# Kernel optimization log

Hardware: AMD Instinct MI355X
Metric: run time of the kernel (lower is better)

The kernel has to match this reference:

```python
import jax, jax.numpy as jnp
import numpy as np

EMB_DIM = 128
HIDDEN = 1024
CL_TEMPERATURE = 0.5
NUM_LABELS = 20
EPS = 1e-14


def setup_inputs() -> dict:
    key = jax.random.key(0)
    k1, k2, k3, k4, k5, k6 = jax.random.split(key, 6)
    B, L = 4, 128
    token_repr = jax.random.normal(k1, (B, L, HIDDEN), dtype=jnp.float32)
    labels = jax.random.randint(k2, (B, L), 0, NUM_LABELS, dtype=jnp.int64)
    mask = jnp.ones((B, L), dtype=jnp.int64)
    # Linear params (PyTorch default init scale ~ U(-1/sqrt(fan_in), 1/sqrt(fan_in)))
    s = 1.0 / np.sqrt(HIDDEN)
    W_mu = jax.random.uniform(k3, (HIDDEN, EMB_DIM), jnp.float32, -s, s)
    b_mu = jax.random.uniform(k4, (EMB_DIM,), jnp.float32, -s, s)
    W_sigma = jax.random.uniform(k5, (HIDDEN, EMB_DIM), jnp.float32, -s, s)
    b_sigma = jax.random.uniform(k6, (EMB_DIM,), jnp.float32, -s, s)
    return {"token_repr": token_repr, "labels": labels, "mask": mask,
            "W_mu": W_mu, "b_mu": b_mu, "W_sigma": W_sigma, "b_sigma": b_sigma}


def _pairwise_sym_kl(mu, sigma):
    """Symmetric diagonal-Gaussian KL between all pairs. mu,sigma: [N,D] -> [N,N]."""
    D = mu.shape[-1]
    mu_i, mu_j = mu[:, None, :], mu[None, :, :]          # [N,N,D] broadcast
    si, sj = sigma[:, None, :], sigma[None, :, :]
    r_ij = sj / si                                        # [N,N,D]
    ij_kl = 0.5 * (r_ij.sum(-1)
                   + (((mu_i - mu_j) ** 2) / si).sum(-1)
                   - D
                   - jnp.log(r_ij + EPS).sum(-1))
    r_ji = si / sj
    ji_kl = 0.5 * (r_ji.sum(-1)
                   + (((mu_j - mu_i) ** 2) / sj).sum(-1)
                   - D
                   - jnp.log(r_ji + EPS).sum(-1))
    return 0.5 * (ij_kl + ji_kl)


def reference(token_repr, labels, mask, W_mu, b_mu, W_sigma, b_sigma):
    h = jax.nn.relu(token_repr)                           # nn.ReLU before Linear
    mu = (h @ W_mu + b_mu).reshape(-1, EMB_DIM)           # [N,D]
    sigma = (jax.nn.elu(h @ W_sigma + b_sigma) + 1.0 + EPS).reshape(-1, EMB_DIM)
    lab = labels.reshape(-1)
    valid = (mask.reshape(-1) == 1) & (lab > 0)           # torch does this by filtering; we mask

    # loss = -symmetric KL for all pairs (cl_type='kl')
    loss = -_pairwise_sym_kl(mu, sigma)                   # [N,N]

    # denominator mask: all embedding dims differ (excludes self / duplicates)
    all_diff = jnp.all(mu[:, None, :] != mu[None, :, :], axis=-1)
    den_mask = all_diff & valid[:, None] & valid[None, :]
    num_mask = den_mask & (lab[:, None] == lab[None, :])

    # NT-Xent with masked reduction; rows with zero positives (or invalid) dropped
    e = jnp.exp(loss / CL_TEMPERATURE)                    # kl >= 0 so e <= 1, stable
    cnts = jnp.sum(num_mask, axis=1).astype(loss.dtype)
    loss_num = jnp.sum(e * num_mask, axis=1)
    loss_den = jnp.sum(e * den_mask, axis=1)
    include = cnts > 0
    safe = lambda x: jnp.where(include, x, 1.0)
    loss_final = -jnp.log(safe(loss_num)) + jnp.log(safe(loss_den)) + jnp.log(safe(cnts))
    n_inc = jnp.maximum(jnp.sum(include), 1).astype(loss.dtype)
    return jnp.sum(jnp.where(include, loss_final, 0.0)) / n_inc
```

## Files before the change

### kernel.cpp

```cpp
#include <hip/hip_runtime.h>
#include <math.h>

#define N_TOK 512
#define DIM   128
#define KDIM  1024
#define EPSF  1e-14f

__global__ __launch_bounds__(512) void projT(
    const float* __restrict__ token, const float* __restrict__ Wmu,
    const float* __restrict__ bmu, const float* __restrict__ Wsg,
    const float* __restrict__ bsg, float* __restrict__ mu,
    float* __restrict__ sg, float* __restrict__ iv,
    float* __restrict__ jmuT, float2* __restrict__ jsviT)
{
    __shared__ float hs[8][KDIM];
    __shared__ float4 red[3][8][16];
    const int bid = blockIdx.x;
    const int t = threadIdx.x;

    const int rowg = bid >> 2, colsel = bid & 3;
    const int m = colsel >> 1, ch = colsel & 1;

    {
        const float4* src = (const float4*)(token + (size_t)rowg * 8 * KDIM);
        float4* dst = (float4*)&hs[0][0];
        #pragma unroll
        for (int r = 0; r < 4; ++r) {
            int idx = t + r * 512;
            float4 v = src[idx];
            v.x = fmaxf(v.x, 0.f); v.y = fmaxf(v.y, 0.f);
            v.z = fmaxf(v.z, 0.f); v.w = fmaxf(v.w, 0.f);
            dst[idx] = v;
        }
    }
    __syncthreads();

    const int q = t & 15, rsub = t >> 4;
    const int row = rsub & 7, kq = rsub >> 3;
    const int d = ch * 64 + q * 4;
    const float* __restrict__ W = (m ? Wsg : Wmu) + (size_t)(kq * 256) * DIM + d;
    const float4* hp = (const float4*)(&hs[row][kq * 256]);

    float4 acc = make_float4(0.f, 0.f, 0.f, 0.f);
    #pragma unroll 4
    for (int k4 = 0; k4 < 64; ++k4) {
        float4 h = hp[k4];
        const float* wp = W + (size_t)(k4 * 4) * DIM;
        float4 w0 = *(const float4*)(wp);
        float4 w1 = *(const float4*)(wp + DIM);
        float4 w2 = *(const float4*)(wp + 2 * DIM);
        float4 w3 = *(const float4*)(wp + 3 * DIM);
        acc.x = fmaf(h.x, w0.x, acc.x); acc.y = fmaf(h.x, w0.y, acc.y);
        acc.z = fmaf(h.x, w0.z, acc.z); acc.w = fmaf(h.x, w0.w, acc.w);
        acc.x = fmaf(h.y, w1.x, acc.x); acc.y = fmaf(h.y, w1.y, acc.y);
        acc.z = fmaf(h.y, w1.z, acc.z); acc.w = fmaf(h.y, w1.w, acc.w);
        acc.x = fmaf(h.z, w2.x, acc.x); acc.y = fmaf(h.z, w2.y, acc.y);
        acc.z = fmaf(h.z, w2.z, acc.z); acc.w = fmaf(h.z, w2.w, acc.w);
        acc.x = fmaf(h.w, w3.x, acc.x); acc.y = fmaf(h.w, w3.y, acc.y);
        acc.z = fmaf(h.w, w3.z, acc.z); acc.w = fmaf(h.w, w3.w, acc.w);
    }

    if (kq > 0) red[kq - 1][row][q] = acc;
    __syncthreads();
    if (kq == 0) {
        float4 r0 = red[0][row][q], r1 = red[1][row][q], r2 = red[2][row][q];
        acc.x += r0.x + r1.x + r2.x; acc.y += r0.y + r1.y + r2.y;
        acc.z += r0.z + r1.z + r2.z; acc.w += r0.w + r1.w + r2.w;
        const int rowi = rowg * 8 + row;
        if (m == 0) {
            float4 b = *(const float4*)(bmu + d);
            acc.x += b.x; acc.y += b.y; acc.z += b.z; acc.w += b.w;
            *(float4*)(mu + (size_t)rowi * DIM + d) = acc;
            jmuT[(size_t)(d + 0) * N_TOK + rowi] = acc.x;
            jmuT[(size_t)(d + 1) * N_TOK + rowi] = acc.y;
            jmuT[(size_t)(d + 2) * N_TOK + rowi] = acc.z;
            jmuT[(size_t)(d + 3) * N_TOK + rowi] = acc.w;
        } else {
            float4 b = *(const float4*)(bsg + d);
            float x0 = acc.x + b.x, x1 = acc.y + b.y;
            float x2 = acc.z + b.z, x3 = acc.w + b.w;
            float4 e, vv;
            e.x = (x0 > 0.f ? x0 : expm1f(x0)) + 1.0f + EPSF;
            e.y = (x1 > 0.f ? x1 : expm1f(x1)) + 1.0f + EPSF;
            e.z = (x2 > 0.f ? x2 : expm1f(x2)) + 1.0f + EPSF;
            e.w = (x3 > 0.f ? x3 : expm1f(x3)) + 1.0f + EPSF;
            vv.x = 1.0f / e.x; vv.y = 1.0f / e.y;
            vv.z = 1.0f / e.z; vv.w = 1.0f / e.w;
            *(float4*)(sg + (size_t)rowi * DIM + d) = e;
            *(float4*)(iv + (size_t)rowi * DIM + d) = vv;
            jsviT[(size_t)(d + 0) * N_TOK + rowi] = make_float2(e.x, vv.x);
            jsviT[(size_t)(d + 1) * N_TOK + rowi] = make_float2(e.y, vv.y);
            jsviT[(size_t)(d + 2) * N_TOK + rowi] = make_float2(e.z, vv.z);
            jsviT[(size_t)(d + 3) * N_TOK + rowi] = make_float2(e.w, vv.w);
        }
    }
}

__global__ __launch_bounds__(256) void pair_kernel(
    const float* __restrict__ mu, const float* __restrict__ sg,
    const float* __restrict__ iv, const float* __restrict__ jmuT,
    const float2* __restrict__ jsviT, const int* __restrict__ labels,
    const int* __restrict__ mask, float* __restrict__ gpart)
{
    __shared__ float si[3][16][DIM];
    __shared__ int slab[16], svalid[16];
    const int ig = blockIdx.x >> 4, jg = blockIdx.x & 15;
    const int i0 = ig * 16, j0 = jg * 32;
    const int t = threadIdx.x;

    #pragma unroll
    for (int rep = 0; rep < 2; ++rep) {
        int f = t + rep * 256;
        int row = f >> 5, kq = f & 31;
        size_t off = (size_t)(i0 + row) * DIM + kq * 4;
        ((float4*)&si[0][0][0])[f] = *(const float4*)(mu + off);
        ((float4*)&si[1][0][0])[f] = *(const float4*)(sg + off);
        ((float4*)&si[2][0][0])[f] = *(const float4*)(iv + off);
    }
    if (t < 16) {
        int lab = labels[i0 + t];
        slab[t] = lab;
        svalid[t] = (mask[i0 + t] == 1 && lab > 0) ? 1 : 0;
    }
    __syncthreads();

    const int jl = t & 31, isub = t >> 5;
    const int ia = 2 * isub, ib = ia + 1;
    const int j = j0 + jl;
    const int labj = labels[j];
    const bool validj = (mask[j] == 1) && (labj > 0);

    const float*  pmT = jmuT  + j;
    const float2* psT = jsviT + j;

    float accA = 0.f, accB = 0.f;
    float mnA = 1e30f, mnB = 1e30f;

    #pragma unroll 4
    for (int q = 0; q < 32; ++q) {
        const int d0 = q * 4;
        float  jm0 = pmT[(size_t)(d0 + 0) * N_TOK];
        float  jm1 = pmT[(size_t)(d0 + 1) * N_TOK];
        float  jm2 = pmT[(size_t)(d0 + 2) * N_TOK];
        float  jm3 = pmT[(size_t)(d0 + 3) * N_TOK];
        float2 sv0 = psT[(size_t)(d0 + 0) * N_TOK];
        float2 sv1 = psT[(size_t)(d0 + 1) * N_TOK];
        float2 sv2 = psT[(size_t)(d0 + 2) * N_TOK];
        float2 sv3 = psT[(size_t)(d0 + 3) * N_TOK];

        float4 bmA = *(const float4*)(&si[0][ia][d0]);
        float4 bsA = *(const float4*)(&si[1][ia][d0]);
        float4 bvA = *(const float4*)(&si[2][ia][d0]);
        float4 bmB = *(const float4*)(&si[0][ib][d0]);
        float4 bsB = *(const float4*)(&si[1][ib][d0]);
        float4 bvB = *(const float4*)(&si[2][ib][d0]);

        float dm;
        dm = bmA.x - jm0; accA = fmaf(fmaf(dm, dm, sv0.x), bvA.x, fmaf(fmaf(dm, dm, bsA.x), sv0.y, accA)); mnA = fminf(mnA, fabsf(dm));
        dm = bmA.y - jm1; accA = fmaf(fmaf(dm, dm, sv1.x), bvA.y, fmaf(fmaf(dm, dm, bsA.y), sv1.y, accA)); mnA = fminf(mnA, fabsf(dm));
        dm = bmA.z - jm2; accA = fmaf(fmaf(dm, dm, sv2.x), bvA.z, fmaf(fmaf(dm, dm, bsA.z), sv2.y, accA)); mnA = fminf(mnA, fabsf(dm));
        dm = bmA.w - jm3; accA = fmaf(fmaf(dm, dm, sv3.x), bvA.w, fmaf(fmaf(dm, dm, bsA.w), sv3.y, accA)); mnA = fminf(mnA, fabsf(dm));

        dm = bmB.x - jm0; accB = fmaf(fmaf(dm, dm, sv0.x), bvB.x, fmaf(fmaf(dm, dm, bsB.x), sv0.y, accB)); mnB = fminf(mnB, fabsf(dm));
        dm = bmB.y - jm1; accB = fmaf(fmaf(dm, dm, sv1.x), bvB.y, fmaf(fmaf(dm, dm, bsB.y), sv1.y, accB)); mnB = fminf(mnB, fabsf(dm));
        dm = bmB.z - jm2; accB = fmaf(fmaf(dm, dm, sv2.x), bvB.z, fmaf(fmaf(dm, dm, bsB.z), sv2.y, accB)); mnB = fminf(mnB, fabsf(dm));
        dm = bmB.w - jm3; accB = fmaf(fmaf(dm, dm, sv3.x), bvB.w, fmaf(fmaf(dm, dm, bsB.w), sv3.y, accB)); mnB = fminf(mnB, fabsf(dm));
    }

    float eA = expf(128.0f - 0.5f * accA);
    float eB = expf(128.0f - 0.5f * accB);
    bool pvA = validj && (svalid[ia] != 0) && (mnA != 0.0f);
    bool pvB = validj && (svalid[ib] != 0) && (mnB != 0.0f);
    bool smA = pvA && (labj == slab[ia]);
    bool smB = pvB && (labj == slab[ib]);
    float dA = pvA ? eA : 0.f, nA = smA ? eA : 0.f, cA = smA ? 1.f : 0.f;
    float dB = pvB ? eB : 0.f, nB = smB ? eB : 0.f, cB = smB ? 1.f : 0.f;

    #pragma unroll
    for (int m = 1; m < 32; m <<= 1) {
        cA += __shfl_xor(cA, m); nA += __shfl_xor(nA, m); dA += __shfl_xor(dA, m);
        cB += __shfl_xor(cB, m); nB += __shfl_xor(nB, m); dB += __shfl_xor(dB, m);
    }
    if (jl == 0) {
        float* pa = gpart + ((size_t)jg * N_TOK + i0 + ia) * 3;
        float* pb = gpart + ((size_t)jg * N_TOK + i0 + ib) * 3;
        pa[0] = cA; pa[1] = nA; pa[2] = dA;
        pb[0] = cB; pb[1] = nB; pb[2] = dB;
    }
}

__global__ __launch_bounds__(512) void final_kernel(
    const float* __restrict__ gpart, float* __restrict__ out)
{
    __shared__ float redL[8], redI[8];
    const int t = threadIdx.x;
    float c = 0.f, nm = 0.f, dn = 0.f;
    #pragma unroll
    for (int jg = 0; jg < 16; ++jg) {
        const float* p = gpart + ((size_t)jg * N_TOK + t) * 3;
        c += p[0]; nm += p[1]; dn += p[2];
    }
    const bool inc = c > 0.5f;
    float lf = inc ? (-logf(nm) + logf(dn) + logf(c)) : 0.f;
    float fi = inc ? 1.f : 0.f;
    #pragma unroll
    for (int m = 1; m < 64; m <<= 1) {
        lf += __shfl_xor(lf, m);
        fi += __shfl_xor(fi, m);
    }
    if ((t & 63) == 0) { redL[t >> 6] = lf; redI[t >> 6] = fi; }
    __syncthreads();
    if (t == 0) {
        float L = 0.f, I = 0.f;
        #pragma unroll
        for (int w = 0; w < 8; ++w) { L += redL[w]; I += redI[w]; }
        out[0] = L / fmaxf(I, 1.0f);
    }
}

extern "C" void kernel_launch(void* const* d_in, const int* in_sizes, int n_in,
                              void* d_out, int out_size, void* d_ws, size_t ws_size,
                              hipStream_t stream) {
    const float* token  = (const float*)d_in[0];
    const int*   labels = (const int*)d_in[1];
    const int*   mask   = (const int*)d_in[2];
    const float* Wmu    = (const float*)d_in[3];
    const float* bmu    = (const float*)d_in[4];
    const float* Wsg    = (const float*)d_in[5];
    const float* bsg    = (const float*)d_in[6];

    float*  ws    = (float*)d_ws;
    float*  mu    = ws;
    float*  sg    = mu + 65536;
    float*  iv    = sg + 65536;
    float*  jmuT  = iv + 65536;
    float2* jsviT = (float2*)(jmuT + 65536);
    float*  gpart = (float*)(jsviT + 65536);

    projT<<<256, 512, 0, stream>>>(token, Wmu, bmu, Wsg, bsg, mu, sg, iv,
                                   jmuT, jsviT);
    pair_kernel<<<512, 256, 0, stream>>>(mu, sg, iv, jmuT, jsviT, labels, mask,
                                         gpart);
    final_kernel<<<1, 512, 0, stream>>>(gpart, (float*)d_out);
}
```

Before: 105.5 us.

## Split projection K across more threads and give each pair thread one i row

The projection kernel now launches 512 blocks, each covering 32 output columns, and splits K into 8 slices of 128 with a 7-way shared-memory reduction. The pair kernel moves to 512 threads per block, with each thread handling a single i row instead of two. Both changes aim for more parallelism and shorter per-thread dependency chains on this small problem. In exchange, the token tile is loaded into shared memory twice as often, the projection reduction is larger, and the pair kernel loses the reuse of each j-column global load across two rows.

```diff
diff --git a/kernel.cpp b/kernel.cpp
--- a/kernel.cpp
+++ b/kernel.cpp
@@ -14,12 +14,12 @@
     float* __restrict__ jmuT, float2* __restrict__ jsviT)
 {
     __shared__ float hs[8][KDIM];
-    __shared__ float4 red[3][8][16];
+    __shared__ float4 red[7][8][8];
     const int bid = blockIdx.x;
     const int t = threadIdx.x;
 
-    const int rowg = bid >> 2, colsel = bid & 3;
-    const int m = colsel >> 1, ch = colsel & 1;
+    const int rowg = bid >> 3, sel = bid & 7;
+    const int m = sel >> 2, ch = sel & 3;
 
     {
         const float4* src = (const float4*)(token + (size_t)rowg * 8 * KDIM);
@@ -35,15 +35,15 @@
     }
     __syncthreads();
 
-    const int q = t & 15, rsub = t >> 4;
+    const int q = t & 7, rsub = t >> 3;
     const int row = rsub & 7, kq = rsub >> 3;
-    const int d = ch * 64 + q * 4;
-    const float* __restrict__ W = (m ? Wsg : Wmu) + (size_t)(kq * 256) * DIM + d;
-    const float4* hp = (const float4*)(&hs[row][kq * 256]);
+    const int d = ch * 32 + q * 4;
+    const float* __restrict__ W = (m ? Wsg : Wmu) + (size_t)(kq * 128) * DIM + d;
+    const float4* hp = (const float4*)(&hs[row][kq * 128]);
 
     float4 acc = make_float4(0.f, 0.f, 0.f, 0.f);
     #pragma unroll 4
-    for (int k4 = 0; k4 < 64; ++k4) {
+    for (int k4 = 0; k4 < 32; ++k4) {
         float4 h = hp[k4];
         const float* wp = W + (size_t)(k4 * 4) * DIM;
         float4 w0 = *(const float4*)(wp);
@@ -63,9 +63,11 @@
     if (kq > 0) red[kq - 1][row][q] = acc;
     __syncthreads();
     if (kq == 0) {
-        float4 r0 = red[0][row][q], r1 = red[1][row][q], r2 = red[2][row][q];
-        acc.x += r0.x + r1.x + r2.x; acc.y += r0.y + r1.y + r2.y;
-        acc.z += r0.z + r1.z + r2.z; acc.w += r0.w + r1.w + r2.w;
+        #pragma unroll
+        for (int s = 0; s < 7; ++s) {
+            float4 r = red[s][row][q];
+            acc.x += r.x; acc.y += r.y; acc.z += r.z; acc.w += r.w;
+        }
         const int rowi = rowg * 8 + row;
         if (m == 0) {
             float4 b = *(const float4*)(bmu + d);
@@ -96,7 +98,7 @@
     }
 }
 
-__global__ __launch_bounds__(256) void pair_kernel(
+__global__ __launch_bounds__(512) void pair_kernel(
     const float* __restrict__ mu, const float* __restrict__ sg,
     const float* __restrict__ iv, const float* __restrict__ jmuT,
     const float2* __restrict__ jsviT, const int* __restrict__ labels,
@@ -108,14 +110,12 @@
     const int i0 = ig * 16, j0 = jg * 32;
     const int t = threadIdx.x;
 
-    #pragma unroll
-    for (int rep = 0; rep < 2; ++rep) {
-        int f = t + rep * 256;
-        int row = f >> 5, kq = f & 31;
+    {
+        int row = t >> 5, kq = t & 31;
         size_t off = (size_t)(i0 + row) * DIM + kq * 4;
-        ((float4*)&si[0][0][0])[f] = *(const float4*)(mu + off);
-        ((float4*)&si[1][0][0])[f] = *(const float4*)(sg + off);
-        ((float4*)&si[2][0][0])[f] = *(const float4*)(iv + off);
+        ((float4*)&si[0][0][0])[t] = *(const float4*)(mu + off);
+        ((float4*)&si[1][0][0])[t] = *(const float4*)(sg + off);
+        ((float4*)&si[2][0][0])[t] = *(const float4*)(iv + off);
     }
     if (t < 16) {
         int lab = labels[i0 + t];
@@ -124,8 +124,7 @@
     }
     __syncthreads();
 
-    const int jl = t & 31, isub = t >> 5;
-    const int ia = 2 * isub, ib = ia + 1;
+    const int jl = t & 31, il = t >> 5;
     const int j = j0 + jl;
     const int labj = labels[j];
     const bool validj = (mask[j] == 1) && (labj > 0);
@@ -133,8 +132,8 @@
     const float*  pmT = jmuT  + j;
     const float2* psT = jsviT + j;
 
-    float accA = 0.f, accB = 0.f;
-    float mnA = 1e30f, mnB = 1e30f;
+    float acc = 0.f;
+    float mn = 1e30f;
 
     #pragma unroll 4
     for (int q = 0; q < 32; ++q) {
@@ -148,44 +147,29 @@
         float2 sv2 = psT[(size_t)(d0 + 2) * N_TOK];
         float2 sv3 = psT[(size_t)(d0 + 3) * N_TOK];
 
-        float4 bmA = *(const float4*)(&si[0][ia][d0]);
-        float4 bsA = *(const float4*)(&si[1][ia][d0]);
-        float4 bvA = *(const float4*)(&si[2][ia][d0]);
-        float4 bmB = *(const float4*)(&si[0][ib][d0]);
-        float4 bsB = *(const float4*)(&si[1][ib][d0]);
-        float4 bvB = *(const float4*)(&si[2][ib][d0]);
+        float4 bm = *(const float4*)(&si[0][il][d0]);
+        float4 bs = *(const float4*)(&si[1][il][d0]);
+        float4 bv = *(const float4*)(&si[2][il][d0]);
 
         float dm;
-        dm = bmA.x - jm0; accA = fmaf(fmaf(dm, dm, sv0.x), bvA.x, fmaf(fmaf(dm, dm, bsA.x), sv0.y, accA)); mnA = fminf(mnA, fabsf(dm));
-        dm = bmA.y - jm1; accA = fmaf(fmaf(dm, dm, sv1.x), bvA.y, fmaf(fmaf(dm, dm, bsA.y), sv1.y, accA)); mnA = fminf(mnA, fabsf(dm));
-        dm = bmA.z - jm2; accA = fmaf(fmaf(dm, dm, sv2.x), bvA.z, fmaf(fmaf(dm, dm, bsA.z), sv2.y, accA)); mnA = fminf(mnA, fabsf(dm));
-        dm = bmA.w - jm3; accA = fmaf(fmaf(dm, dm, sv3.x), bvA.w, fmaf(fmaf(dm, dm, bsA.w), sv3.y, accA)); mnA = fminf(mnA, fabsf(dm));
-
-        dm = bmB.x - jm0; accB = fmaf(fmaf(dm, dm, sv0.x), bvB.x, fmaf(fmaf(dm, dm, bsB.x), sv0.y, accB)); mnB = fminf(mnB, fabsf(dm));
-        dm = bmB.y - jm1; accB = fmaf(fmaf(dm, dm, sv1.x), bvB.y, fmaf(fmaf(dm, dm, bsB.y), sv1.y, accB)); mnB = fminf(mnB, fabsf(dm));
-        dm = bmB.z - jm2; accB = fmaf(fmaf(dm, dm, sv2.x), bvB.z, fmaf(fmaf(dm, dm, bsB.z), sv2.y, accB)); mnB = fminf(mnB, fabsf(dm));
-        dm = bmB.w - jm3; accB = fmaf(fmaf(dm, dm, sv3.x), bvB.w, fmaf(fmaf(dm, dm, bsB.w), sv3.y, accB)); mnB = fminf(mnB, fabsf(dm));
-    }
-
-    float eA = expf(128.0f - 0.5f * accA);
-    float eB = expf(128.0f - 0.5f * accB);
-    bool pvA = validj && (svalid[ia] != 0) && (mnA != 0.0f);
-    bool pvB = validj && (svalid[ib] != 0) && (mnB != 0.0f);
-    bool smA = pvA && (labj == slab[ia]);
-    bool smB = pvB && (labj == slab[ib]);
-    float dA = pvA ? eA : 0.f, nA = smA ? eA : 0.f, cA = smA ? 1.f : 0.f;
-    float dB = pvB ? eB : 0.f, nB = smB ? eB : 0.f, cB = smB ? 1.f : 0.f;
+        dm = bm.x - jm0; acc = fmaf(fmaf(dm, dm, sv0.x), bv.x, fmaf(fmaf(dm, dm, bs.x), sv0.y, acc)); mn = fminf(mn, fabsf(dm));
+        dm = bm.y - jm1; acc = fmaf(fmaf(dm, dm, sv1.x), bv.y, fmaf(fmaf(dm, dm, bs.y), sv1.y, acc)); mn = fminf(mn, fabsf(dm));
+        dm = bm.z - jm2; acc = fmaf(fmaf(dm, dm, sv2.x), bv.z, fmaf(fmaf(dm, dm, bs.z), sv2.y, acc)); mn = fminf(mn, fabsf(dm));
+        dm = bm.w - jm3; acc = fmaf(fmaf(dm, dm, sv3.x), bv.w, fmaf(fmaf(dm, dm, bs.w), sv3.y, acc)); mn = fminf(mn, fabsf(dm));
+    }
+
+    float e = expf(128.0f - 0.5f * acc);
+    bool pv = validj && (svalid[il] != 0) && (mn != 0.0f);
+    bool sm = pv && (labj == slab[il]);
+    float dd = pv ? e : 0.f, nn = sm ? e : 0.f, cc = sm ? 1.f : 0.f;
 
     #pragma unroll
     for (int m = 1; m < 32; m <<= 1) {
-        cA += __shfl_xor(cA, m); nA += __shfl_xor(nA, m); dA += __shfl_xor(dA, m);
-        cB += __shfl_xor(cB, m); nB += __shfl_xor(nB, m); dB += __shfl_xor(dB, m);
+        cc += __shfl_xor(cc, m); nn += __shfl_xor(nn, m); dd += __shfl_xor(dd, m);
     }
     if (jl == 0) {
-        float* pa = gpart + ((size_t)jg * N_TOK + i0 + ia) * 3;
-        float* pb = gpart + ((size_t)jg * N_TOK + i0 + ib) * 3;
-        pa[0] = cA; pa[1] = nA; pa[2] = dA;
-        pb[0] = cB; pb[1] = nB; pb[2] = dB;
+        float* pa = gpart + ((size_t)jg * N_TOK + i0 + il) * 3;
+        pa[0] = cc; pa[1] = nn; pa[2] = dd;
     }
 }
 
@@ -237,9 +221,9 @@
     float2* jsviT = (float2*)(jmuT + 65536);
     float*  gpart = (float*)(jsviT + 65536);
 
-    projT<<<256, 512, 0, stream>>>(token, Wmu, bmu, Wsg, bsg, mu, sg, iv,
+    projT<<<512, 512, 0, stream>>>(token, Wmu, bmu, Wsg, bsg, mu, sg, iv,
                                    jmuT, jsviT);
-    pair_kernel<<<512, 256, 0, stream>>>(mu, sg, iv, jmuT, jsviT, labels, mask,
+    pair_kernel<<<512, 512, 0, stream>>>(mu, sg, iv, jmuT, jsviT, labels, mask,
                                          gpart);
     final_kernel<<<1, 512, 0, stream>>>(gpart, (float*)d_out);
 }
```

New measurement: 109.6 us. 1.04x slower.
